# Performance work log

Hardware: AMD Instinct MI355X
Metric: run time of the kernel (lower is better)

## Reference

```python
import jax, jax.numpy as jnp
import numpy as np

HEADS = 8
DIM_HEAD = 32
SCALE = DIM_HEAD ** -0.5


def _split_heads(t):
    # [b, n, h*d] -> [b, h, n, d]
    b, n, hd = t.shape
    return t.reshape(b, n, HEADS, hd // HEADS).transpose(0, 2, 1, 3)


def setup_inputs() -> dict:
    key = jax.random.key(0)
    k1, k2, k3, k4 = jax.random.split(key, 4)
    b, n, dim = 2, 2048, 256
    inner = HEADS * DIM_HEAD  # 256
    x = jax.random.normal(k1, (b, n, dim), dtype=jnp.float32)
    attn_feat = jax.random.normal(k2, (b, n, dim), dtype=jnp.float32)
    # nn.Linear(dim, 3*inner, bias=False): store as [dim, 3*inner] for x @ W
    W_qkv = jax.random.normal(k3, (dim, 3 * inner), dtype=jnp.float32) * (dim ** -0.5)
    W_qkv_aux = jax.random.normal(k4, (dim, 3 * inner), dtype=jnp.float32) * (dim ** -0.5)
    return {"x": x, "attn_feat": attn_feat, "W_qkv": W_qkv, "W_qkv_aux": W_qkv_aux,
            "use_cls_tokens": 1}


def reference(x, attn_feat, W_qkv, W_qkv_aux, use_cls_tokens):
    b, n, dim = x.shape
    # aux Q,K (v_aux computed but unused, matching original chunk of 3)
    qkv_aux = attn_feat @ W_qkv_aux            # [b, n, 3*inner]
    q_aux, k_aux, _ = jnp.split(qkv_aux, 3, axis=-1)
    q_aux, k_aux = _split_heads(q_aux), _split_heads(k_aux)
    # self Q,K
    qkv_self = x @ W_qkv
    q_self, k_self, _ = jnp.split(qkv_self, 3, axis=-1)
    q_self, k_self = _split_heads(q_self), _split_heads(k_self)
    # dual score product: (QK^T_aux * scale) * (QK^T_self * scale)
    dots_aux = jnp.einsum('bhid,bhjd->bhij', q_aux, k_aux) * SCALE
    dots_self = jnp.einsum('bhid,bhjd->bhij', q_self, k_self) * SCALE
    attn = jax.nn.softmax(dots_aux * dots_self, axis=-1)  # [b, h, n, n]
    # v = x.unsqueeze(1): broadcast raw x over heads
    out = jnp.einsum('bhij,bjd->bhid', attn, x)           # [b, h, n, dim]
    out = out.transpose(0, 2, 1, 3).reshape(b, n, HEADS * dim)
    attn_flat = attn.transpose(0, 2, 1, 3).reshape(b, n, HEADS * n)
    return (out, out[:, 0], attn_flat[:, 0])
```

## Files before the change

### kernel.cpp

```cpp
#include <hip/hip_runtime.h>

typedef _Float16 f16;
typedef _Float16 f16x4 __attribute__((ext_vector_type(4)));
typedef _Float16 f16x8 __attribute__((ext_vector_type(8)));
typedef float f32x4 __attribute__((ext_vector_type(4)));

#define LOG2E 1.4426950408889634f
#define SCL   (1.4426950408889634f / 32.0f)

__global__ __launch_bounds__(256) void k_transpose(const float* __restrict__ x,
                                                   f16* __restrict__ xt) {
  __shared__ f16 tile[64][65];
  int n0 = blockIdx.x * 64;
  int d0 = blockIdx.y * 64;
  int b  = blockIdx.z;
  int t = threadIdx.x;
  int colr = t & 63, rowg = t >> 6;
#pragma unroll
  for (int r = 0; r < 16; ++r) {
    int row = r * 4 + rowg;
    tile[row][colr] = (f16)x[((size_t)b * 2048 + n0 + row) * 256 + d0 + colr];
  }
  __syncthreads();
#pragma unroll
  for (int r = 0; r < 16; ++r) {
    int drow = r * 4 + rowg;
    xt[((size_t)b * 256 + d0 + drow) * 2048 + n0 + colr] = tile[colr][drow];
  }
}

__global__ __launch_bounds__(256) void k_transW(const float* __restrict__ Wq,
    const float* __restrict__ Wa, f16* __restrict__ Wt) {
  __shared__ f16 tile[64][65];
  int n0 = blockIdx.x * 64, k0 = blockIdx.y * 64, s = blockIdx.z;
  const float* W = s ? Wa : Wq;
  f16* dst = Wt + (size_t)s * 512 * 256;
  int t = threadIdx.x, c = t & 63, rg = t >> 6;
#pragma unroll
  for (int r = 0; r < 16; ++r) {
    int krow = r * 4 + rg;
    tile[krow][c] = (f16)W[(size_t)(k0 + krow) * 768 + n0 + c];
  }
  __syncthreads();
#pragma unroll
  for (int r = 0; r < 16; ++r) {
    int nrow = r * 4 + rg;
    dst[(size_t)(n0 + nrow) * 256 + k0 + c] = tile[c][nrow];
  }
}

__global__ __launch_bounds__(256) void k_proj(const float* __restrict__ x,
    const float* __restrict__ af, const f16* __restrict__ Wt,
    f16* __restrict__ Qs, f16* __restrict__ Ks,
    f16* __restrict__ Qa, f16* __restrict__ Ka) {
  int mt = blockIdx.x, nt = blockIdx.y, s = blockIdx.z;
  const float* A = s ? af : x;
  const f16* W = Wt + (size_t)s * 512 * 256;
  f16* Qd = s ? Qa : Qs;
  f16* Kd = s ? Ka : Ks;
  int t = threadIdx.x, wv = t >> 6, ln = t & 63, cl = ln & 15, g = ln >> 4;
  int m0 = mt * 64, n0 = nt * 64;
  const float* arow = A + (size_t)(m0 + wv * 16 + cl) * 256 + g * 8;
  const f16* wb = W + (size_t)n0 * 256 + g * 8;
  f32x4 z4 = {0.f, 0.f, 0.f, 0.f};
  f32x4 acc[4] = {z4, z4, z4, z4};
#pragma unroll
  for (int k32 = 0; k32 < 8; ++k32) {
    float4 u = *(const float4*)(arow + k32 * 32);
    float4 v = *(const float4*)(arow + k32 * 32 + 4);
    f16x8 a = { (f16)u.x, (f16)u.y, (f16)u.z, (f16)u.w,
                (f16)v.x, (f16)v.y, (f16)v.z, (f16)v.w };
#pragma unroll
    for (int n4 = 0; n4 < 4; ++n4) {
      f16x8 bf = *(const f16x8*)(wb + (size_t)(n4 * 16 + cl) * 256 + k32 * 32);
      acc[n4] = __builtin_amdgcn_mfma_f32_16x16x32_f16(a, bf, acc[n4], 0, 0, 0);
    }
  }
#pragma unroll
  for (int n4 = 0; n4 < 4; ++n4) {
    int c = n0 + n4 * 16 + cl;
    int head = (c & 255) >> 5, d = c & 31;
    f16* dst = (c < 256) ? Qd : Kd;
#pragma unroll
    for (int r = 0; r < 4; ++r) {
      int m = m0 + wv * 16 + g * 4 + r;
      int bb = m >> 11, nn = m & 2047;
      dst[(((size_t)bb * 8 + head) * 2048 + nn) * 32 + d] = (f16)acc[n4][r];
    }
  }
}

__global__ __launch_bounds__(256) void k_flash(const f16* __restrict__ Qs,
    const f16* __restrict__ Ks, const f16* __restrict__ Qa,
    const f16* __restrict__ Ka, const f16* __restrict__ xt,
    float* __restrict__ out, float* __restrict__ out_cls) {
  __shared__ f16 KaL[2][64][40];
  __shared__ f16 KsL[2][64][40];
  __shared__ f16 PL[2][64][72];
  __shared__ float alphaL[2][64];
  __shared__ float lL[64];
  int qt = blockIdx.x, h = blockIdx.y, b = blockIdx.z;
  int bh = b * 8 + h;
  int t = threadIdx.x, wv = t >> 6, ln = t & 63, cl = ln & 15, g = ln >> 4;
  int qrow0 = qt * 64 + wv * 16;
  f16x8 qsf = *(const f16x8*)&Qs[((size_t)bh * 2048 + qrow0 + cl) * 32 + g * 8];
  f16x8 qaf = *(const f16x8*)&Qa[((size_t)bh * 2048 + qrow0 + cl) * 32 + g * 8];
  f32x4 z4 = {0.f, 0.f, 0.f, 0.f};
  f32x4 acc[4][4];
#pragma unroll
  for (int i = 0; i < 4; ++i)
#pragma unroll
    for (int j = 0; j < 4; ++j) acc[i][j] = z4;
  float m_run = -3.0e38f, l_run = 0.f;
  int krow = t >> 2, koff = (t & 3) * 8;
  const f16* kaSrc = Ka + ((size_t)bh * 2048 + krow) * 32 + koff;
  const f16* ksSrc = Ks + ((size_t)bh * 2048 + krow) * 32 + koff;
  const f16* xb = xt + ((size_t)b * 256 + wv * 64) * 2048;

  *(f16x8*)&KaL[0][krow][koff] = *(const f16x8*)kaSrc;
  *(f16x8*)&KsL[0][krow][koff] = *(const f16x8*)ksSrc;
  __syncthreads();

  for (int kt = 0; kt < 32; ++kt) {
    int buf = kt & 1;
    f16x8 kan, ksn;
    if (kt < 31) {
      kan = *(const f16x8*)(kaSrc + (size_t)(kt + 1) * 2048);
      ksn = *(const f16x8*)(ksSrc + (size_t)(kt + 1) * 2048);
    }
    f16x8 xf[2][4];
#pragma unroll
    for (int ks2 = 0; ks2 < 2; ++ks2)
#pragma unroll
      for (int ddt = 0; ddt < 4; ++ddt)
        xf[ks2][ddt] = *(const f16x8*)(xb + (size_t)(ddt * 16 + cl) * 2048 +
                                       kt * 64 + ks2 * 32 + g * 8);
    float p[16];
    float tmax = -3.0e38f;
#pragma unroll
    for (int jt = 0; jt < 4; ++jt) {
      f16x8 kaf = *(const f16x8*)&KaL[buf][jt * 16 + cl][g * 8];
      f16x8 ksf = *(const f16x8*)&KsL[buf][jt * 16 + cl][g * 8];
      f32x4 za = __builtin_amdgcn_mfma_f32_16x16x32_f16(kaf, qaf, z4, 0, 0, 0);
      f32x4 zs = __builtin_amdgcn_mfma_f32_16x16x32_f16(ksf, qsf, z4, 0, 0, 0);
#pragma unroll
      for (int r = 0; r < 4; ++r) {
        float sv = za[r] * zs[r] * SCL;
        p[jt * 4 + r] = sv;
        tmax = fmaxf(tmax, sv);
      }
    }
    tmax = fmaxf(tmax, __shfl_xor(tmax, 16, 64));
    tmax = fmaxf(tmax, __shfl_xor(tmax, 32, 64));
    float m_new = fmaxf(m_run, tmax);
    float alpha = exp2f(m_run - m_new);
    float lsum = 0.f;
#pragma unroll
    for (int q = 0; q < 16; ++q) {
      p[q] = exp2f(p[q] - m_new);
      lsum += p[q];
    }
    lsum += __shfl_xor(lsum, 16, 64);
    lsum += __shfl_xor(lsum, 32, 64);
    l_run = l_run * alpha + lsum;
    m_run = m_new;
    if (kt < 31) {
      *(f16x8*)&KaL[buf ^ 1][krow][koff] = kan;
      *(f16x8*)&KsL[buf ^ 1][krow][koff] = ksn;
    }
#pragma unroll
    for (int jt = 0; jt < 4; ++jt) {
      f16x4 pk = { (f16)p[jt * 4 + 0], (f16)p[jt * 4 + 1],
                   (f16)p[jt * 4 + 2], (f16)p[jt * 4 + 3] };
      *(f16x4*)&PL[buf][wv * 16 + cl][jt * 16 + g * 4] = pk;
    }
    if (g == 0) alphaL[buf][wv * 16 + cl] = alpha;
    __syncthreads();
    float av[4][4];
    int need = 0;
#pragma unroll
    for (int qt2 = 0; qt2 < 4; ++qt2)
#pragma unroll
      for (int r = 0; r < 4; ++r) {
        float a = alphaL[buf][qt2 * 16 + g * 4 + r];
        av[qt2][r] = a;
        need |= (a != 1.0f);
      }
    if (__any(need)) {
#pragma unroll
      for (int qt2 = 0; qt2 < 4; ++qt2)
#pragma unroll
        for (int ddt = 0; ddt < 4; ++ddt)
#pragma unroll
          for (int r = 0; r < 4; ++r) acc[qt2][ddt][r] *= av[qt2][r];
    }
#pragma unroll
    for (int ks2 = 0; ks2 < 2; ++ks2) {
      f16x8 pf[4];
#pragma unroll
      for (int qt2 = 0; qt2 < 4; ++qt2)
        pf[qt2] = *(const f16x8*)&PL[buf][qt2 * 16 + cl][ks2 * 32 + g * 8];
#pragma unroll
      for (int ddt = 0; ddt < 4; ++ddt)
#pragma unroll
        for (int qt2 = 0; qt2 < 4; ++qt2)
          acc[qt2][ddt] = __builtin_amdgcn_mfma_f32_16x16x32_f16(
              pf[qt2], xf[ks2][ddt], acc[qt2][ddt], 0, 0, 0);
    }
  }
  if (g == 0) lL[wv * 16 + cl] = l_run;
  __syncthreads();
#pragma unroll
  for (int qt2 = 0; qt2 < 4; ++qt2) {
#pragma unroll
    for (int r = 0; r < 4; ++r) {
      float linv = 1.0f / lL[qt2 * 16 + g * 4 + r];
      int q = qt * 64 + qt2 * 16 + g * 4 + r;
#pragma unroll
      for (int ddt = 0; ddt < 4; ++ddt) {
        float v = acc[qt2][ddt][r] * linv;
        int col = h * 256 + wv * 64 + ddt * 16 + cl;
        out[((size_t)b * 2048 + q) * 2048 + col] = v;
        if (q == 0) out_cls[(size_t)b * 2048 + col] = v;
      }
    }
  }
}

__global__ __launch_bounds__(256) void k_attn0(const f16* __restrict__ Qs,
    const f16* __restrict__ Ks, const f16* __restrict__ Qa,
    const f16* __restrict__ Ka, float* __restrict__ dst) {
  __shared__ float qa_s[32], qs_s[32];
  __shared__ float red[256];
  int h = blockIdx.x, b = blockIdx.y, bh = b * 8 + h;
  int t = threadIdx.x;
  if (t < 32) {
    qa_s[t] = (float)Qa[(size_t)bh * 2048 * 32 + t];
    qs_s[t] = (float)Qs[(size_t)bh * 2048 * 32 + t];
  }
  __syncthreads();
  float sv[8];
#pragma unroll
  for (int r = 0; r < 8; ++r) {
    int j = r * 256 + t;
    const f16x8* ka8 = (const f16x8*)&Ka[((size_t)bh * 2048 + j) * 32];
    const f16x8* ks8 = (const f16x8*)&Ks[((size_t)bh * 2048 + j) * 32];
    float da = 0.f, ds = 0.f;
#pragma unroll
    for (int c = 0; c < 4; ++c) {
      f16x8 va = ka8[c], vs = ks8[c];
#pragma unroll
      for (int d = 0; d < 8; ++d) {
        da += qa_s[c * 8 + d] * (float)va[d];
        ds += qs_s[c * 8 + d] * (float)vs[d];
      }
    }
    sv[r] = da * ds * (1.f / 32.f);
  }
  float mx = sv[0];
#pragma unroll
  for (int r = 1; r < 8; ++r) mx = fmaxf(mx, sv[r]);
  red[t] = mx;
  __syncthreads();
  for (int st = 128; st > 0; st >>= 1) {
    if (t < st) red[t] = fmaxf(red[t], red[t + st]);
    __syncthreads();
  }
  float m = red[0];
  __syncthreads();
  float e[8], sum = 0.f;
#pragma unroll
  for (int r = 0; r < 8; ++r) {
    e[r] = exp2f((sv[r] - m) * LOG2E);
    sum += e[r];
  }
  red[t] = sum;
  __syncthreads();
  for (int st = 128; st > 0; st >>= 1) {
    if (t < st) red[t] += red[t + st];
    __syncthreads();
  }
  float l = red[0];
#pragma unroll
  for (int r = 0; r < 8; ++r)
    dst[(size_t)b * 16384 + h * 2048 + r * 256 + t] = e[r] / l;
}

extern "C" void kernel_launch(void* const* d_in, const int* in_sizes, int n_in,
                              void* d_out, int out_size, void* d_ws, size_t ws_size,
                              hipStream_t stream) {
  const float* x  = (const float*)d_in[0];
  const float* af = (const float*)d_in[1];
  const float* Wq = (const float*)d_in[2];
  const float* Wa = (const float*)d_in[3];
  const size_t QK = (size_t)2 * 8 * 2048 * 32;
  f16* Qs = (f16*)d_ws;
  f16* Ks = Qs + QK;
  f16* Qa = Ks + QK;
  f16* Ka = Qa + QK;
  f16* xt = Ka + QK;
  f16* Wt = xt + QK;
  float* out     = (float*)d_out;
  float* out_cls = out + (size_t)2 * 2048 * 2048;
  float* attn0   = out_cls + 2 * 2048;

  k_transpose<<<dim3(32, 4, 2), 256, 0, stream>>>(x, xt);
  k_transW<<<dim3(8, 4, 2), 256, 0, stream>>>(Wq, Wa, Wt);
  k_proj<<<dim3(64, 8, 2), 256, 0, stream>>>(x, af, Wt, Qs, Ks, Qa, Ka);
  k_flash<<<dim3(32, 8, 2), 256, 0, stream>>>(Qs, Ks, Qa, Ka, xt, out, out_cls);
  k_attn0<<<dim3(8, 2), 256, 0, stream>>>(Qs, Ks, Qa, Ka, attn0);
}
```

Measured before the change: 187.8 us.

## Merge transposes, loop proj over N tiles, fold scale, fuse attn0 into flash

```diff
diff --git a/kernel.cpp b/kernel.cpp
--- a/kernel.cpp
+++ b/kernel.cpp
@@ -5,47 +5,42 @@
 typedef _Float16 f16x8 __attribute__((ext_vector_type(8)));
 typedef float f32x4 __attribute__((ext_vector_type(4)));
 
-#define LOG2E 1.4426950408889634f
-#define SCL   (1.4426950408889634f / 32.0f)
-
-__global__ __launch_bounds__(256) void k_transpose(const float* __restrict__ x,
-                                                   f16* __restrict__ xt) {
+#define SCL (1.4426950408889634f / 32.0f)
+
+__global__ __launch_bounds__(256) void k_stage(const float* __restrict__ x,
+    const float* __restrict__ Wq, const float* __restrict__ Wa,
+    f16* __restrict__ xt, f16* __restrict__ Wt) {
   __shared__ f16 tile[64][65];
-  int n0 = blockIdx.x * 64;
-  int d0 = blockIdx.y * 64;
-  int b  = blockIdx.z;
-  int t = threadIdx.x;
-  int colr = t & 63, rowg = t >> 6;
-#pragma unroll
-  for (int r = 0; r < 16; ++r) {
-    int row = r * 4 + rowg;
-    tile[row][colr] = (f16)x[((size_t)b * 2048 + n0 + row) * 256 + d0 + colr];
-  }
-  __syncthreads();
-#pragma unroll
-  for (int r = 0; r < 16; ++r) {
-    int drow = r * 4 + rowg;
-    xt[((size_t)b * 256 + d0 + drow) * 2048 + n0 + colr] = tile[colr][drow];
-  }
-}
-
-__global__ __launch_bounds__(256) void k_transW(const float* __restrict__ Wq,
-    const float* __restrict__ Wa, f16* __restrict__ Wt) {
-  __shared__ f16 tile[64][65];
-  int n0 = blockIdx.x * 64, k0 = blockIdx.y * 64, s = blockIdx.z;
-  const float* W = s ? Wa : Wq;
-  f16* dst = Wt + (size_t)s * 512 * 256;
+  int bx = blockIdx.x;
   int t = threadIdx.x, c = t & 63, rg = t >> 6;
-#pragma unroll
-  for (int r = 0; r < 16; ++r) {
-    int krow = r * 4 + rg;
-    tile[krow][c] = (f16)W[(size_t)(k0 + krow) * 768 + n0 + c];
-  }
-  __syncthreads();
-#pragma unroll
-  for (int r = 0; r < 16; ++r) {
-    int nrow = r * 4 + rg;
-    dst[(size_t)(n0 + nrow) * 256 + k0 + c] = tile[c][nrow];
+  if (bx < 32) {
+    int n0 = bx * 64, d0 = blockIdx.y * 64, b = blockIdx.z;
+#pragma unroll
+    for (int r = 0; r < 16; ++r) {
+      int row = r * 4 + rg;
+      tile[row][c] = (f16)x[((size_t)b * 2048 + n0 + row) * 256 + d0 + c];
+    }
+    __syncthreads();
+#pragma unroll
+    for (int r = 0; r < 16; ++r) {
+      int drow = r * 4 + rg;
+      xt[((size_t)b * 256 + d0 + drow) * 2048 + n0 + c] = tile[c][drow];
+    }
+  } else {
+    int n0 = (bx - 32) * 64, k0 = blockIdx.y * 64, s = blockIdx.z;
+    const float* W = s ? Wa : Wq;
+    f16* dst = Wt + (size_t)s * 512 * 256;
+#pragma unroll
+    for (int r = 0; r < 16; ++r) {
+      int krow = r * 4 + rg;
+      tile[krow][c] = (f16)W[(size_t)(k0 + krow) * 768 + n0 + c];
+    }
+    __syncthreads();
+#pragma unroll
+    for (int r = 0; r < 16; ++r) {
+      int nrow = r * 4 + rg;
+      dst[(size_t)(n0 + nrow) * 256 + k0 + c] = tile[c][nrow];
+    }
   }
 }
 
@@ -53,39 +48,47 @@
     const float* __restrict__ af, const f16* __restrict__ Wt,
     f16* __restrict__ Qs, f16* __restrict__ Ks,
     f16* __restrict__ Qa, f16* __restrict__ Ka) {
-  int mt = blockIdx.x, nt = blockIdx.y, s = blockIdx.z;
+  int mt = blockIdx.x, s = blockIdx.y;
   const float* A = s ? af : x;
   const f16* W = Wt + (size_t)s * 512 * 256;
   f16* Qd = s ? Qa : Qs;
   f16* Kd = s ? Ka : Ks;
   int t = threadIdx.x, wv = t >> 6, ln = t & 63, cl = ln & 15, g = ln >> 4;
-  int m0 = mt * 64, n0 = nt * 64;
+  int m0 = mt * 64;
   const float* arow = A + (size_t)(m0 + wv * 16 + cl) * 256 + g * 8;
-  const f16* wb = W + (size_t)n0 * 256 + g * 8;
-  f32x4 z4 = {0.f, 0.f, 0.f, 0.f};
-  f32x4 acc[4] = {z4, z4, z4, z4};
+  f16x8 a[8];
 #pragma unroll
   for (int k32 = 0; k32 < 8; ++k32) {
     float4 u = *(const float4*)(arow + k32 * 32);
     float4 v = *(const float4*)(arow + k32 * 32 + 4);
-    f16x8 a = { (f16)u.x, (f16)u.y, (f16)u.z, (f16)u.w,
-                (f16)v.x, (f16)v.y, (f16)v.z, (f16)v.w };
+    a[k32] = (f16x8){ (f16)u.x, (f16)u.y, (f16)u.z, (f16)u.w,
+                      (f16)v.x, (f16)v.y, (f16)v.z, (f16)v.w };
+  }
+  f32x4 z4 = {0.f, 0.f, 0.f, 0.f};
+#pragma unroll 1
+  for (int nt = 0; nt < 8; ++nt) {
+    int n0 = nt * 64;
+    f32x4 acc[4] = {z4, z4, z4, z4};
+    const f16* wb = W + (size_t)n0 * 256 + g * 8;
+#pragma unroll
+    for (int k32 = 0; k32 < 8; ++k32)
+#pragma unroll
+      for (int n4 = 0; n4 < 4; ++n4) {
+        f16x8 bf = *(const f16x8*)(wb + (size_t)(n4 * 16 + cl) * 256 + k32 * 32);
+        acc[n4] = __builtin_amdgcn_mfma_f32_16x16x32_f16(a[k32], bf, acc[n4], 0, 0, 0);
+      }
 #pragma unroll
     for (int n4 = 0; n4 < 4; ++n4) {
-      f16x8 bf = *(const f16x8*)(wb + (size_t)(n4 * 16 + cl) * 256 + k32 * 32);
-      acc[n4] = __builtin_amdgcn_mfma_f32_16x16x32_f16(a, bf, acc[n4], 0, 0, 0);
-    }
-  }
-#pragma unroll
-  for (int n4 = 0; n4 < 4; ++n4) {
-    int c = n0 + n4 * 16 + cl;
-    int head = (c & 255) >> 5, d = c & 31;
-    f16* dst = (c < 256) ? Qd : Kd;
-#pragma unroll
-    for (int r = 0; r < 4; ++r) {
-      int m = m0 + wv * 16 + g * 4 + r;
-      int bb = m >> 11, nn = m & 2047;
-      dst[(((size_t)bb * 8 + head) * 2048 + nn) * 32 + d] = (f16)acc[n4][r];
+      int c = n0 + n4 * 16 + cl;
+      int head = (c & 255) >> 5, d = c & 31;
+      f16* dst = (c < 256) ? Qd : Kd;
+      float osc = (s && (n0 + n4 * 16) >= 256) ? SCL : 1.0f;
+#pragma unroll
+      for (int r = 0; r < 4; ++r) {
+        int m = m0 + wv * 16 + g * 4 + r;
+        int bb = m >> 11, nn = m & 2047;
+        dst[(((size_t)bb * 8 + head) * 2048 + nn) * 32 + d] = (f16)(acc[n4][r] * osc);
+      }
     }
   }
 }
@@ -93,11 +96,13 @@
 __global__ __launch_bounds__(256) void k_flash(const f16* __restrict__ Qs,
     const f16* __restrict__ Ks, const f16* __restrict__ Qa,
     const f16* __restrict__ Ka, const f16* __restrict__ xt,
-    float* __restrict__ out, float* __restrict__ out_cls) {
+    float* __restrict__ out, float* __restrict__ out_cls,
+    float* __restrict__ attn0, float* __restrict__ lq0) {
   __shared__ f16 KaL[2][64][40];
   __shared__ f16 KsL[2][64][40];
   __shared__ f16 PL[2][64][72];
-  __shared__ float alphaL[2][64];
+  __shared__ float alphaL[2][64] __attribute__((aligned(16)));
+  __shared__ int   flagS[2][4]  __attribute__((aligned(16)));
   __shared__ float lL[64];
   int qt = blockIdx.x, h = blockIdx.y, b = blockIdx.z;
   int bh = b * 8 + h;
@@ -111,30 +116,38 @@
   for (int i = 0; i < 4; ++i)
 #pragma unroll
     for (int j = 0; j < 4; ++j) acc[i][j] = z4;
-  float m_run = -3.0e38f, l_run = 0.f;
+  float m_run = -3.0e38f;
+  float l_run = 0.f;
   int krow = t >> 2, koff = (t & 3) * 8;
-  const f16* kaSrc = Ka + ((size_t)bh * 2048 + krow) * 32 + koff;
-  const f16* ksSrc = Ks + ((size_t)bh * 2048 + krow) * 32 + koff;
+  const f16* kaP = Ka + ((size_t)bh * 2048 + krow) * 32 + koff;
+  const f16* ksP = Ks + ((size_t)bh * 2048 + krow) * 32 + koff;
   const f16* xb = xt + ((size_t)b * 256 + wv * 64) * 2048;
-
-  *(f16x8*)&KaL[0][krow][koff] = *(const f16x8*)kaSrc;
-  *(f16x8*)&KsL[0][krow][koff] = *(const f16x8*)ksSrc;
+  const f16* xp[4];
+#pragma unroll
+  for (int ddt = 0; ddt < 4; ++ddt)
+    xp[ddt] = xb + (size_t)(ddt * 16 + cl) * 2048 + g * 8;
+  float* a0p = attn0 + (size_t)b * 16384 + h * 2048;
+
+  *(f16x8*)&KaL[0][krow][koff] = *(const f16x8*)kaP;
+  *(f16x8*)&KsL[0][krow][koff] = *(const f16x8*)ksP;
+  kaP += 2048; ksP += 2048;
   __syncthreads();
 
   for (int kt = 0; kt < 32; ++kt) {
     int buf = kt & 1;
     f16x8 kan, ksn;
     if (kt < 31) {
-      kan = *(const f16x8*)(kaSrc + (size_t)(kt + 1) * 2048);
-      ksn = *(const f16x8*)(ksSrc + (size_t)(kt + 1) * 2048);
+      kan = *(const f16x8*)kaP;
+      ksn = *(const f16x8*)ksP;
+      kaP += 2048; ksP += 2048;
     }
     f16x8 xf[2][4];
 #pragma unroll
-    for (int ks2 = 0; ks2 < 2; ++ks2)
-#pragma unroll
-      for (int ddt = 0; ddt < 4; ++ddt)
-        xf[ks2][ddt] = *(const f16x8*)(xb + (size_t)(ddt * 16 + cl) * 2048 +
-                                       kt * 64 + ks2 * 32 + g * 8);
+    for (int ddt = 0; ddt < 4; ++ddt) {
+      xf[0][ddt] = *(const f16x8*)(xp[ddt]);
+      xf[1][ddt] = *(const f16x8*)(xp[ddt] + 32);
+      xp[ddt] += 64;
+    }
     float p[16];
     float tmax = -3.0e38f;
 #pragma unroll
@@ -145,54 +158,58 @@
       f32x4 zs = __builtin_amdgcn_mfma_f32_16x16x32_f16(ksf, qsf, z4, 0, 0, 0);
 #pragma unroll
       for (int r = 0; r < 4; ++r) {
-        float sv = za[r] * zs[r] * SCL;
+        float sv = za[r] * zs[r];
         p[jt * 4 + r] = sv;
         tmax = fmaxf(tmax, sv);
       }
     }
     tmax = fmaxf(tmax, __shfl_xor(tmax, 16, 64));
     tmax = fmaxf(tmax, __shfl_xor(tmax, 32, 64));
-    float m_new = fmaxf(m_run, tmax);
-    float alpha = exp2f(m_run - m_new);
+    bool upd = tmax > m_run;
+    float m_new = upd ? tmax + 6.0f : m_run;
+    float alpha = upd ? exp2f(m_run - m_new) : 1.0f;
+    if (qt == 0 && wv == 0 && cl == 0) {
+#pragma unroll
+      for (int jt = 0; jt < 4; ++jt) {
+        float4 v = { p[jt * 4 + 0], p[jt * 4 + 1], p[jt * 4 + 2], p[jt * 4 + 3] };
+        *(float4*)(a0p + kt * 64 + jt * 16 + g * 4) = v;
+      }
+    }
     float lsum = 0.f;
 #pragma unroll
     for (int q = 0; q < 16; ++q) {
       p[q] = exp2f(p[q] - m_new);
       lsum += p[q];
     }
-    lsum += __shfl_xor(lsum, 16, 64);
-    lsum += __shfl_xor(lsum, 32, 64);
     l_run = l_run * alpha + lsum;
     m_run = m_new;
     if (kt < 31) {
       *(f16x8*)&KaL[buf ^ 1][krow][koff] = kan;
       *(f16x8*)&KsL[buf ^ 1][krow][koff] = ksn;
     }
+    if (g == 0) alphaL[buf][wv * 16 + cl] = alpha;
+    unsigned long long blt = __ballot(upd);
+    if (ln == 0) flagS[buf][wv] = (blt != 0ull) ? 1 : 0;
 #pragma unroll
     for (int jt = 0; jt < 4; ++jt) {
       f16x4 pk = { (f16)p[jt * 4 + 0], (f16)p[jt * 4 + 1],
                    (f16)p[jt * 4 + 2], (f16)p[jt * 4 + 3] };
       *(f16x4*)&PL[buf][wv * 16 + cl][jt * 16 + g * 4] = pk;
     }
-    if (g == 0) alphaL[buf][wv * 16 + cl] = alpha;
     __syncthreads();
-    float av[4][4];
-    int need = 0;
-#pragma unroll
-    for (int qt2 = 0; qt2 < 4; ++qt2)
-#pragma unroll
-      for (int r = 0; r < 4; ++r) {
-        float a = alphaL[buf][qt2 * 16 + g * 4 + r];
-        av[qt2][r] = a;
-        need |= (a != 1.0f);
-      }
-    if (__any(need)) {
-#pragma unroll
-      for (int qt2 = 0; qt2 < 4; ++qt2)
-#pragma unroll
-        for (int ddt = 0; ddt < 4; ++ddt)
-#pragma unroll
-          for (int r = 0; r < 4; ++r) acc[qt2][ddt][r] *= av[qt2][r];
+    int4 fl = *(const int4*)&flagS[buf][0];
+    if (fl.x | fl.y | fl.z | fl.w) {
+#pragma unroll
+      for (int qt2 = 0; qt2 < 4; ++qt2) {
+        float4 av = *(const float4*)&alphaL[buf][qt2 * 16 + g * 4];
+#pragma unroll
+        for (int ddt = 0; ddt < 4; ++ddt) {
+          acc[qt2][ddt][0] *= av.x;
+          acc[qt2][ddt][1] *= av.y;
+          acc[qt2][ddt][2] *= av.z;
+          acc[qt2][ddt][3] *= av.w;
+        }
+      }
     }
 #pragma unroll
     for (int ks2 = 0; ks2 < 2; ++ks2) {
@@ -208,7 +225,10 @@
               pf[qt2], xf[ks2][ddt], acc[qt2][ddt], 0, 0, 0);
     }
   }
+  l_run += __shfl_xor(l_run, 16, 64);
+  l_run += __shfl_xor(l_run, 32, 64);
   if (g == 0) lL[wv * 16 + cl] = l_run;
+  if (qt == 0 && t == 0) { lq0[bh * 2] = l_run; lq0[bh * 2 + 1] = m_run; }
   __syncthreads();
 #pragma unroll
   for (int qt2 = 0; qt2 < 4; ++qt2) {
@@ -227,63 +247,18 @@
   }
 }
 
-__global__ __launch_bounds__(256) void k_attn0(const f16* __restrict__ Qs,
-    const f16* __restrict__ Ks, const f16* __restrict__ Qa,
-    const f16* __restrict__ Ka, float* __restrict__ dst) {
-  __shared__ float qa_s[32], qs_s[32];
-  __shared__ float red[256];
+__global__ __launch_bounds__(256) void k_norm0(float* __restrict__ attn0,
+                                               const float* __restrict__ lq0) {
   int h = blockIdx.x, b = blockIdx.y, bh = b * 8 + h;
+  float linv = 1.0f / lq0[bh * 2];
+  float m0 = lq0[bh * 2 + 1];
+  float* p = attn0 + (size_t)b * 16384 + h * 2048;
   int t = threadIdx.x;
-  if (t < 32) {
-    qa_s[t] = (float)Qa[(size_t)bh * 2048 * 32 + t];
-    qs_s[t] = (float)Qs[(size_t)bh * 2048 * 32 + t];
-  }
-  __syncthreads();
-  float sv[8];
 #pragma unroll
   for (int r = 0; r < 8; ++r) {
-    int j = r * 256 + t;
-    const f16x8* ka8 = (const f16x8*)&Ka[((size_t)bh * 2048 + j) * 32];
-    const f16x8* ks8 = (const f16x8*)&Ks[((size_t)bh * 2048 + j) * 32];
-    float da = 0.f, ds = 0.f;
-#pragma unroll
-    for (int c = 0; c < 4; ++c) {
-      f16x8 va = ka8[c], vs = ks8[c];
-#pragma unroll
-      for (int d = 0; d < 8; ++d) {
-        da += qa_s[c * 8 + d] * (float)va[d];
-        ds += qs_s[c * 8 + d] * (float)vs[d];
-      }
-    }
-    sv[r] = da * ds * (1.f / 32.f);
-  }
-  float mx = sv[0];
-#pragma unroll
-  for (int r = 1; r < 8; ++r) mx = fmaxf(mx, sv[r]);
-  red[t] = mx;
-  __syncthreads();
-  for (int st = 128; st > 0; st >>= 1) {
-    if (t < st) red[t] = fmaxf(red[t], red[t + st]);
-    __syncthreads();
-  }
-  float m = red[0];
-  __syncthreads();
-  float e[8], sum = 0.f;
-#pragma unroll
-  for (int r = 0; r < 8; ++r) {
-    e[r] = exp2f((sv[r] - m) * LOG2E);
-    sum += e[r];
-  }
-  red[t] = sum;
-  __syncthreads();
-  for (int st = 128; st > 0; st >>= 1) {
-    if (t < st) red[t] += red[t + st];
-    __syncthreads();
-  }
-  float l = red[0];
-#pragma unroll
-  for (int r = 0; r < 8; ++r)
-    dst[(size_t)b * 16384 + h * 2048 + r * 256 + t] = e[r] / l;
+    float s = p[r * 256 + t];
+    p[r * 256 + t] = exp2f(s - m0) * linv;
+  }
 }
 
 extern "C" void kernel_launch(void* const* d_in, const int* in_sizes, int n_in,
@@ -300,13 +275,14 @@
   f16* Ka = Qa + QK;
   f16* xt = Ka + QK;
   f16* Wt = xt + QK;
+  float* lq0 = (float*)(Wt + (size_t)2 * 512 * 256);
   float* out     = (float*)d_out;
   float* out_cls = out + (size_t)2 * 2048 * 2048;
   float* attn0   = out_cls + 2 * 2048;
 
-  k_transpose<<<dim3(32, 4, 2), 256, 0, stream>>>(x, xt);
-  k_transW<<<dim3(8, 4, 2), 256, 0, stream>>>(Wq, Wa, Wt);
-  k_proj<<<dim3(64, 8, 2), 256, 0, stream>>>(x, af, Wt, Qs, Ks, Qa, Ka);
-  k_flash<<<dim3(32, 8, 2), 256, 0, stream>>>(Qs, Ks, Qa, Ka, xt, out, out_cls);
-  k_attn0<<<dim3(8, 2), 256, 0, stream>>>(Qs, Ks, Qa, Ka, attn0);
-}
+  k_stage<<<dim3(40, 4, 2), 256, 0, stream>>>(x, Wq, Wa, xt, Wt);
+  k_proj<<<dim3(64, 2), 256, 0, stream>>>(x, af, Wt, Qs, Ks, Qa, Ka);
+  k_flash<<<dim3(32, 8, 2), 256, 0, stream>>>(Qs, Ks, Qa, Ka, xt, out, out_cls,
+                                              attn0, lq0);
+  k_norm0<<<dim3(8, 2), 256, 0, stream>>>(attn0, lq0);
+}
```

After: 264.8 us. 1.41x slower.
